# Kernel tuning notes

Measured on AMD Instinct MI355X. Metric: run time of the kernel, lower is better.

## Reference

```python
import jax, jax.numpy as jnp
import numpy as np

B, D = 4096, 1024
N_CLASSES = 100
INF = jnp.float32(3.4e38)


def setup_inputs() -> dict:
    key = jax.random.key(0)
    k1, k2 = jax.random.split(key)
    x = jax.random.normal(k1, (B, 1, D), dtype=jnp.float32)
    labels = jax.random.randint(k2, (B,), 0, N_CLASSES)
    return {"x": x, "labels": labels}


def _awareness_scan(xs, labels_f, R_init):
    # xs: [B, D] float32, labels_f: [B] float32
    b, d = xs.shape
    slots = jnp.arange(b)

    def step(state, inp):
        refs, ref_labels, n_refs, count, min_d, max_d, R = state
        xi, li = inp
        mask = slots < n_refs  # active reference slots
        # distances from candidate to current reference set (torch.cdist, p=2)
        d_all = jnp.sqrt(jnp.sum((refs - xi[None, :]) ** 2, axis=-1))  # [B]
        d_all = jax.lax.stop_gradient(d_all)
        d_act = jnp.where(mask, d_all, INF)
        min_act = jnp.min(d_act)
        is_first = count == 1
        # new reference iff ALL active distances exceed R (i.e. min > R)
        insert = is_first | (min_act > R)
        refs2 = jnp.where(insert, refs.at[n_refs].set(xi), refs)
        ref_labels2 = jnp.where(insert, ref_labels.at[n_refs].set(li), ref_labels)
        n_refs2 = n_refs + insert.astype(n_refs.dtype)
        # dynamic ray update (skipped on the very first sample, as in torch)
        max_act = jnp.max(jnp.where(mask, d_all, -INF))
        min_d2 = jnp.where(is_first, min_d, jnp.minimum(min_d, min_act))
        max_d2 = jnp.where(is_first, max_d, jnp.maximum(max_d, max_act))
        R2 = jnp.where(is_first, R, (min_d2 + max_d2) / 3)
        # prediction: nearest reference AFTER potential insertion
        mask2 = slots < n_refs2
        d2 = jnp.sqrt(jnp.sum((refs2 - xi[None, :]) ** 2, axis=-1))
        d2 = jax.lax.stop_gradient(d2)
        idx = jnp.argmin(jnp.where(mask2, d2, INF))
        pred = ref_labels2[idx]
        new_state = (refs2, ref_labels2, n_refs2, count + 1, min_d2, max_d2, R2)
        return new_state, pred

    init = (
        jnp.zeros((b, d), jnp.float32),   # reference instances buffer
        jnp.zeros((b,), jnp.float32),     # reference labels buffer
        jnp.int32(0),                     # n_refs
        jnp.int32(1),                     # count (starts at 1, as in torch)
        INF,                              # min_dist
        jnp.float32(0.0),                 # max_dist
        jnp.float32(R_init),              # R
    )
    _, preds = jax.lax.scan(step, init, (xs, labels_f))
    return preds  # [B] float32


def reference(x, labels):
    # x: [B, 1, D]; labels: [B] int. update_ref_insts=True, set_labels=labels.
    xs = x.reshape(x.shape[0], x.shape[2])
    labels_f = labels.astype(jnp.float32)
    return _awareness_scan(xs, labels_f, 1.0)
```

## Files before the change

### kernel.cpp

```cpp
#include <hip/hip_runtime.h>
#include <stdint.h>

#define B_N   4096
#define D_DIM 1024
#define INF_F 3.4e38f

typedef __bf16 bf16x8 __attribute__((ext_vector_type(8)));
typedef float  floatx4 __attribute__((ext_vector_type(4)));

#define XBF_OFF 131072

__device__ inline unsigned short f2bf_rne(float f) {
    unsigned u = __float_as_uint(f);
    unsigned r = (u + 0x7FFFu + ((u >> 16) & 1u)) >> 16;
    return (unsigned short)r;
}

__global__ __launch_bounds__(256)
void k_prep(const float* __restrict__ x, unsigned short* __restrict__ xbf,
            float* __restrict__ norms,
            unsigned long long* __restrict__ minpack,
            unsigned int* __restrict__ maxbits) {
    const int row = blockIdx.x;
    const int t   = threadIdx.x;
    float4 v = ((const float4*)x)[row * 256 + t];
    ushort4 o;
    o.x = f2bf_rne(v.x); o.y = f2bf_rne(v.y);
    o.z = f2bf_rne(v.z); o.w = f2bf_rne(v.w);
    ((ushort4*)xbf)[row * 256 + t] = o;
    float s = v.x * v.x + v.y * v.y + v.z * v.z + v.w * v.w;
    #pragma unroll
    for (int off = 32; off; off >>= 1) s += __shfl_down(s, off);
    __shared__ float ws4[4];
    if ((t & 63) == 0) ws4[t >> 6] = s;
    __syncthreads();
    if (t == 0) {
        norms[row]   = ws4[0] + ws4[1] + ws4[2] + ws4[3];
        minpack[row] = 0xFFFFFFFFFFFFFFFFull;
        maxbits[row] = 0u;
    }
}

#define GLDS(g, l)                                                              \
    __builtin_amdgcn_global_load_lds(                                           \
        (__attribute__((address_space(1))) void*)(void*)(g),                    \
        (__attribute__((address_space(3))) void*)(void*)(l), 16, 0, 0)

__global__ __launch_bounds__(256, 3)
void k_pass1_mfma(const unsigned short* __restrict__ xbf,
                  const float* __restrict__ norms,
                  unsigned long long* __restrict__ minpack,
                  unsigned int* __restrict__ maxbits) {
    int bid = blockIdx.x;
    int ti  = (int)((sqrtf(8.f * bid + 1.f) - 1.f) * 0.5f);
    while ((ti + 1) * (ti + 2) / 2 <= bid) ti++;
    while (ti * (ti + 1) / 2 > bid) ti--;
    int tj  = bid - ti * (ti + 1) / 2;

    __shared__ unsigned short As[2][4096];
    __shared__ unsigned short Bs[2][4096];
    __shared__ unsigned long long redMin[128][2];
    __shared__ float redMax[128][2];

    const int t    = threadIdx.x;
    const int w    = t >> 6, lane = t & 63;
    const int wm   = w >> 1, wn = w & 1;
    const int q4   = lane >> 4, c15 = lane & 15;
    const int i0   = ti * 128, j0 = tj * 128;

    const int sr = lane >> 2;
    const int sc = ((lane & 3) + 4 - (lane >> 4)) & 3;

    const unsigned short* gA[2]; const unsigned short* gB[2];
    unsigned short* lA[2][2]; unsigned short* lB[2][2];
    #pragma unroll
    for (int q = 0; q < 2; q++) {
        int e   = w * 2 + q;
        int row = e * 16 + sr;
        gA[q] = xbf + (size_t)(i0 + row) * D_DIM + sc * 8;
        gB[q] = xbf + (size_t)(j0 + row) * D_DIM + sc * 8;
        #pragma unroll
        for (int b = 0; b < 2; b++) {
            lA[b][q] = &As[b][e * 512];
            lB[b][q] = &Bs[b][e * 512];
        }
    }

    int aoff[4], boff[4];
    #pragma unroll
    for (int st = 0; st < 4; st++) {
        int sw = ((q4 + (c15 >> 2)) & 3) << 4;
        aoff[st] = (wm * 4 + st) * 1024 + c15 * 64 + sw;
        boff[st] = (wn * 4 + st) * 1024 + c15 * 64 + sw;
    }

    floatx4 acc[4][4];
    #pragma unroll
    for (int m = 0; m < 4; m++)
        #pragma unroll
        for (int n = 0; n < 4; n++)
            acc[m][n] = (floatx4){0.f, 0.f, 0.f, 0.f};

    #pragma unroll
    for (int q = 0; q < 2; q++) { GLDS(gA[q], lA[0][q]); GLDS(gB[q], lB[0][q]); }

    for (int it = 0; it < 32; it++) {
        __syncthreads();
        if (it < 31) {
            const int nb = (it + 1) & 1;
            #pragma unroll
            for (int q = 0; q < 2; q++) {
                gA[q] += 32; gB[q] += 32;
                GLDS(gA[q], lA[nb][q]);
                GLDS(gB[q], lB[nb][q]);
            }
        }
        const unsigned short* Ac = As[it & 1];
        const unsigned short* Bc = Bs[it & 1];
        bf16x8 af[4], bfr[4];
        #pragma unroll
        for (int st = 0; st < 4; st++) {
            af[st]  = *(const bf16x8*)((const char*)Ac + aoff[st]);
            bfr[st] = *(const bf16x8*)((const char*)Bc + boff[st]);
        }
        #pragma unroll
        for (int m = 0; m < 4; m++)
            #pragma unroll
            for (int n = 0; n < 4; n++)
                acc[m][n] = __builtin_amdgcn_mfma_f32_16x16x32_bf16(
                    af[m], bfr[n], acc[m][n], 0, 0, 0);
    }

    float nj[4];
    #pragma unroll
    for (int st = 0; st < 4; st++) nj[st] = norms[j0 + wn * 64 + st * 16 + c15];

    #pragma unroll
    for (int st_m = 0; st_m < 4; st_m++) {
        #pragma unroll
        for (int r = 0; r < 4; r++) {
            int i_loc = wm * 64 + st_m * 16 + q4 * 4 + r;
            int gi    = i0 + i_loc;
            float ni  = norms[gi];
            unsigned long long mp = 0xFFFFFFFFFFFFFFFFull;
            float mx = -INF_F;
            #pragma unroll
            for (int st_n = 0; st_n < 4; st_n++) {
                int gj = j0 + wn * 64 + st_n * 16 + c15;
                if (gj < gi) {
                    float dot = acc[st_m][st_n][r];
                    float d   = sqrtf(fmaxf(ni + nj[st_n] - 2.f * dot, 0.f));
                    unsigned long long p =
                        ((unsigned long long)__float_as_uint(d) << 32) | (unsigned)gj;
                    if (p < mp) mp = p;
                    mx = fmaxf(mx, d);
                }
            }
            #pragma unroll
            for (int off = 1; off < 16; off <<= 1) {
                unsigned long long op = __shfl_xor(mp, off, 64);
                if (op < mp) mp = op;
                float om = __shfl_xor(mx, off, 64);
                mx = fmaxf(mx, om);
            }
            if (c15 == 0) { redMin[i_loc][wn] = mp; redMax[i_loc][wn] = mx; }
        }
    }
    __syncthreads();
    if (t < 128) {
        unsigned long long mp = redMin[t][0];
        if (redMin[t][1] < mp) mp = redMin[t][1];
        float mx = fmaxf(redMax[t][0], redMax[t][1]);
        if (mp != 0xFFFFFFFFFFFFFFFFull) {
            atomicMin(&minpack[i0 + t], mp);
            atomicMax(&maxbits[i0 + t], __float_as_uint(mx));
        }
    }
}

__global__ __launch_bounds__(1024)
void k_tail(const unsigned long long* __restrict__ minpack,
            const unsigned int* __restrict__ maxbits,
            const float* __restrict__ x, const float* __restrict__ norms,
            const int* __restrict__ labels, int* __restrict__ ref_idx,
            float* __restrict__ out) {
    const int t = threadIdx.x;
    float m[4], M[4];
    #pragma unroll
    for (int q = 0; q < 4; q++) {
        int i = t * 4 + q;
        unsigned long long p = minpack[i];
        float dmin = (p == 0xFFFFFFFFFFFFFFFFull)
                       ? INF_F : __uint_as_float((unsigned)(p >> 32));
        m[q] = (i == 0) ? INF_F : dmin;
        M[q] = (i == 0) ? -INF_F : __uint_as_float(maxbits[i]);
    }
    float pmin[4], pmax[4];
    pmin[0] = m[0]; pmax[0] = M[0];
    #pragma unroll
    for (int q = 1; q < 4; q++) {
        pmin[q] = fminf(pmin[q - 1], m[q]);
        pmax[q] = fmaxf(pmax[q - 1], M[q]);
    }
    __shared__ float smin[1024], smax[1024];
    smin[t] = pmin[3]; smax[t] = pmax[3];
    __syncthreads();
    for (int off = 1; off < 1024; off <<= 1) {
        float a = (t >= off) ? smin[t - off] : INF_F;
        float b = (t >= off) ? smax[t - off] : -INF_F;
        __syncthreads();
        smin[t] = fminf(smin[t], a);
        smax[t] = fmaxf(smax[t], b);
        __syncthreads();
    }
    float exMin = (t > 0) ? smin[t - 1] : INF_F;
    float exMax = (t > 0) ? smax[t - 1] : -INF_F;

    int viol = B_N;
    #pragma unroll
    for (int q = 0; q < 4; q++) {
        int i = t * 4 + q;
        if (i >= 1) {
            float pm = (q == 0) ? exMin : fminf(exMin, pmin[q - 1]);
            float pM = (q == 0) ? exMax : fmaxf(exMax, pmax[q - 1]);
            float R  = (i == 1) ? 1.0f : (pm + pM) / 3.0f;
            if (!(m[q] > R) && i < viol) viol = i;
        }
    }
    __shared__ int sv[1024];
    sv[t] = viol;
    __syncthreads();
    for (int off = 512; off; off >>= 1) {
        if (t < off) sv[t] = min(sv[t], sv[t + off]);
        __syncthreads();
    }
    const int s_star = sv[0];

    for (int i = t; i < s_star; i += 1024) out[i] = (float)labels[i];

    __shared__ float s_state[3];
    __shared__ int s_n;
    if (s_star < B_N && t == (s_star >> 2)) {
        int q = s_star & 3;
        float pm = (q == 0) ? exMin : fminf(exMin, pmin[q - 1]);
        float pM = (q == 0) ? exMax : fmaxf(exMax, pmax[q - 1]);
        float md = fminf(pm, m[q]);
        float Md = fmaxf(pM, M[q]);
        s_state[0] = md; s_state[1] = Md; s_state[2] = (md + Md) / 3.0f;
        s_n = s_star;
        unsigned long long p = minpack[s_star];
        int j = (int)(unsigned)(p & 0xFFFFFFFFu);
        out[s_star] = (float)labels[j];
    }
    if (s_star >= B_N) return;

    for (int s = t; s < s_star; s += 1024) ref_idx[s] = s;
    __syncthreads();

    __shared__ unsigned long long redp[1024];
    __shared__ float redm[1024];
    for (int i = s_star + 1; i < B_N; i++) {
        int n = s_n;
        const float* xi = x + (size_t)i * D_DIM;
        float ni = norms[i];
        unsigned long long mp = 0xFFFFFFFFFFFFFFFFull;
        float mx = -INF_F;
        for (int slot = t; slot < n; slot += 1024) {
            int j = ref_idx[slot];
            const float* xj = x + (size_t)j * D_DIM;
            float dot = 0.f;
            for (int k = 0; k < D_DIM; k++) dot = fmaf(xi[k], xj[k], dot);
            float d = sqrtf(fmaxf(ni + norms[j] - 2.f * dot, 0.f));
            unsigned long long p =
                ((unsigned long long)__float_as_uint(d) << 32) | (unsigned)slot;
            if (p < mp) mp = p;
            mx = fmaxf(mx, d);
        }
        redp[t] = mp; redm[t] = mx;
        __syncthreads();
        for (int off = 512; off; off >>= 1) {
            if (t < off) {
                if (redp[t + off] < redp[t]) redp[t] = redp[t + off];
                redm[t] = fmaxf(redm[t], redm[t + off]);
            }
            __syncthreads();
        }
        if (t == 0) {
            unsigned long long p = redp[0];
            float min_act = __uint_as_float((unsigned)(p >> 32));
            int minslot   = (int)(unsigned)(p & 0xFFFFFFFFu);
            float max_act = redm[0];
            bool insert = (min_act > s_state[2]);
            int pred;
            if (insert) {
                ref_idx[n] = i;
                s_n = n + 1;
                pred = (min_act <= 0.0f) ? labels[ref_idx[minslot]] : labels[i];
            } else {
                pred = labels[ref_idx[minslot]];
            }
            float md = fminf(s_state[0], min_act);
            float Md = fmaxf(s_state[1], max_act);
            s_state[0] = md; s_state[1] = Md; s_state[2] = (md + Md) / 3.0f;
            out[i] = (float)pred;
        }
        __syncthreads();
    }
}

extern "C" void kernel_launch(void* const* d_in, const int* in_sizes, int n_in,
                              void* d_out, int out_size, void* d_ws, size_t ws_size,
                              hipStream_t stream) {
    const float* x      = (const float*)d_in[0];
    const int*   labels = (const int*)d_in[1];
    float*       out    = (float*)d_out;
    char* ws = (char*)d_ws;
    unsigned long long* minpack = (unsigned long long*)ws;
    unsigned int*       maxbits = (unsigned int*)(ws + 32768);
    float*              norms   = (float*)(ws + 49152);
    int*                ref_idx = (int*)(ws + 65600);
    unsigned short*     xbf     = (unsigned short*)(ws + XBF_OFF);

    k_prep<<<B_N, 256, 0, stream>>>(x, xbf, norms, minpack, maxbits);
    const int ntiles  = B_N / 128;
    const int nblocks = ntiles * (ntiles + 1) / 2;
    k_pass1_mfma<<<nblocks, 256, 0, stream>>>(xbf, norms, minpack, maxbits);
    k_tail<<<1, 1024, 0, stream>>>(minpack, maxbits, x, norms, labels, ref_idx, out);
}
```

Measured before the change: 111.4 us.

## Load MFMA operands directly from global memory into registers, dropping LDS staging

The pairwise Gram-matrix kernel no longer stages 128x32 bf16 tiles through double-buffered shared memory via global_load_lds. Each wave now loads its own A/B fragments straight from global memory into registers, with a two-stage software pipeline, and the per-iteration __syncthreads is gone. This removes LDS traffic and barriers, but A/B rows are re-fetched by multiple waves (relying on L1/L2), the loads are strided per lane, and occupancy drops from 3 to 2 blocks per SM.

Result: slower. 170.2 us (+52.7%).

```diff
diff --git a/kernel.cpp b/kernel.cpp
--- a/kernel.cpp
+++ b/kernel.cpp
@@ -41,24 +41,17 @@
     }
 }
 
-#define GLDS(g, l)                                                              \
-    __builtin_amdgcn_global_load_lds(                                           \
-        (__attribute__((address_space(1))) void*)(void*)(g),                    \
-        (__attribute__((address_space(3))) void*)(void*)(l), 16, 0, 0)
-
-__global__ __launch_bounds__(256, 3)
-void k_pass1_mfma(const unsigned short* __restrict__ xbf,
-                  const float* __restrict__ norms,
-                  unsigned long long* __restrict__ minpack,
-                  unsigned int* __restrict__ maxbits) {
+__global__ __launch_bounds__(256, 2)
+void k_pass1_reg(const unsigned short* __restrict__ xbf,
+                 const float* __restrict__ norms,
+                 unsigned long long* __restrict__ minpack,
+                 unsigned int* __restrict__ maxbits) {
     int bid = blockIdx.x;
     int ti  = (int)((sqrtf(8.f * bid + 1.f) - 1.f) * 0.5f);
     while ((ti + 1) * (ti + 2) / 2 <= bid) ti++;
     while (ti * (ti + 1) / 2 > bid) ti--;
     int tj  = bid - ti * (ti + 1) / 2;
 
-    __shared__ unsigned short As[2][4096];
-    __shared__ unsigned short Bs[2][4096];
     __shared__ unsigned long long redMin[128][2];
     __shared__ float redMax[128][2];
 
@@ -68,30 +61,13 @@
     const int q4   = lane >> 4, c15 = lane & 15;
     const int i0   = ti * 128, j0 = tj * 128;
 
-    const int sr = lane >> 2;
-    const int sc = ((lane & 3) + 4 - (lane >> 4)) & 3;
-
-    const unsigned short* gA[2]; const unsigned short* gB[2];
-    unsigned short* lA[2][2]; unsigned short* lB[2][2];
-    #pragma unroll
-    for (int q = 0; q < 2; q++) {
-        int e   = w * 2 + q;
-        int row = e * 16 + sr;
-        gA[q] = xbf + (size_t)(i0 + row) * D_DIM + sc * 8;
-        gB[q] = xbf + (size_t)(j0 + row) * D_DIM + sc * 8;
-        #pragma unroll
-        for (int b = 0; b < 2; b++) {
-            lA[b][q] = &As[b][e * 512];
-            lB[b][q] = &Bs[b][e * 512];
-        }
-    }
-
-    int aoff[4], boff[4];
+    const bf16x8* pA[4]; const bf16x8* pB[4];
     #pragma unroll
     for (int st = 0; st < 4; st++) {
-        int sw = ((q4 + (c15 >> 2)) & 3) << 4;
-        aoff[st] = (wm * 4 + st) * 1024 + c15 * 64 + sw;
-        boff[st] = (wn * 4 + st) * 1024 + c15 * 64 + sw;
+        pA[st] = (const bf16x8*)(xbf +
+                 (size_t)(i0 + wm * 64 + st * 16 + c15) * D_DIM + q4 * 8);
+        pB[st] = (const bf16x8*)(xbf +
+                 (size_t)(j0 + wn * 64 + st * 16 + c15) * D_DIM + q4 * 8);
     }
 
     floatx4 acc[4][4];
@@ -101,34 +77,37 @@
         for (int n = 0; n < 4; n++)
             acc[m][n] = (floatx4){0.f, 0.f, 0.f, 0.f};
 
-    #pragma unroll
-    for (int q = 0; q < 2; q++) { GLDS(gA[q], lA[0][q]); GLDS(gB[q], lB[0][q]); }
-
-    for (int it = 0; it < 32; it++) {
-        __syncthreads();
-        if (it < 31) {
-            const int nb = (it + 1) & 1;
-            #pragma unroll
-            for (int q = 0; q < 2; q++) {
-                gA[q] += 32; gB[q] += 32;
-                GLDS(gA[q], lA[nb][q]);
-                GLDS(gB[q], lB[nb][q]);
-            }
-        }
-        const unsigned short* Ac = As[it & 1];
-        const unsigned short* Bc = Bs[it & 1];
-        bf16x8 af[4], bfr[4];
-        #pragma unroll
-        for (int st = 0; st < 4; st++) {
-            af[st]  = *(const bf16x8*)((const char*)Ac + aoff[st]);
-            bfr[st] = *(const bf16x8*)((const char*)Bc + boff[st]);
+    bf16x8 a0[4], b0[4], a1[4], b1[4];
+    #pragma unroll
+    for (int st = 0; st < 4; st++) { a0[st] = pA[st][0]; b0[st] = pB[st][0]; }
+
+    for (int it = 0; it < 32; it += 2) {
+        if (it + 1 < 32) {
+            #pragma unroll
+            for (int st = 0; st < 4; st++) {
+                a1[st] = pA[st][(it + 1) * 4];
+                b1[st] = pB[st][(it + 1) * 4];
+            }
         }
         #pragma unroll
         for (int m = 0; m < 4; m++)
             #pragma unroll
             for (int n = 0; n < 4; n++)
                 acc[m][n] = __builtin_amdgcn_mfma_f32_16x16x32_bf16(
-                    af[m], bfr[n], acc[m][n], 0, 0, 0);
+                    a0[m], b0[n], acc[m][n], 0, 0, 0);
+        if (it + 2 < 32) {
+            #pragma unroll
+            for (int st = 0; st < 4; st++) {
+                a0[st] = pA[st][(it + 2) * 4];
+                b0[st] = pB[st][(it + 2) * 4];
+            }
+        }
+        #pragma unroll
+        for (int m = 0; m < 4; m++)
+            #pragma unroll
+            for (int n = 0; n < 4; n++)
+                acc[m][n] = __builtin_amdgcn_mfma_f32_16x16x32_bf16(
+                    a1[m], b1[n], acc[m][n], 0, 0, 0);
     }
 
     float nj[4];
@@ -324,6 +303,6 @@
     k_prep<<<B_N, 256, 0, stream>>>(x, xbf, norms, minpack, maxbits);
     const int ntiles  = B_N / 128;
     const int nblocks = ntiles * (ntiles + 1) / 2;
-    k_pass1_mfma<<<nblocks, 256, 0, stream>>>(xbf, norms, minpack, maxbits);
+    k_pass1_reg<<<nblocks, 256, 0, stream>>>(xbf, norms, minpack, maxbits);
     k_tail<<<1, 1024, 0, stream>>>(minpack, maxbits, x, norms, labels, ref_idx, out);
 }
```
